# Kernel optimization log

Hardware: AMD Instinct MI355X
Metric: run time of the kernel (lower is better)

Reference implementation:

```python
import jax, jax.numpy as jnp
import numpy as np

B, L, D = 8, 1024, 512
H, Qd = 8, 64  # heads, per-head dim (q == v == 64)


def setup_inputs() -> dict:
    key = jax.random.key(0)
    ks = jax.random.split(key, 12)
    s = 0.02
    return {
        "x": jax.random.normal(ks[0], (B, L, D), dtype=jnp.float32),
        # Conv1d(D, D, kernel_size=1) == pointwise linear over channels
        "Wc": jax.random.normal(ks[1], (D, D), dtype=jnp.float32) * s,
        "bc": jax.random.normal(ks[2], (D,), dtype=jnp.float32) * s,
        "Wq": jax.random.normal(ks[3], (H * Qd, D), dtype=jnp.float32) * s,
        "bq": jax.random.normal(ks[4], (H * Qd,), dtype=jnp.float32) * s,
        "Wk": jax.random.normal(ks[5], (H * Qd, D), dtype=jnp.float32) * s,
        "bk": jax.random.normal(ks[6], (H * Qd,), dtype=jnp.float32) * s,
        "Wv": jax.random.normal(ks[7], (H * Qd, D), dtype=jnp.float32) * s,
        "bv": jax.random.normal(ks[8], (H * Qd,), dtype=jnp.float32) * s,
        "Wo": jax.random.normal(ks[9], (D, H * Qd), dtype=jnp.float32) * s,
        "bo": jax.random.normal(ks[10], (D,), dtype=jnp.float32) * s,
    }


def reference(x, Wc, bc, Wq, bq, Wk, bk, Wv, bv, Wo, bo):
    b, l, d = x.shape
    # kernel-size-1 Conv1d over channel dim == per-position linear
    x_r = jnp.einsum('bld,od->blo', x, Wc) + bc  # [B, L, D], Lr == L
    Q = (x @ Wq.T + bq).reshape(b, l, H, Qd).transpose(0, 2, 1, 3)    # bhld
    K = (x_r @ Wk.T + bk).reshape(b, l, H, Qd).transpose(0, 2, 1, 3)  # bhjd
    V = (x_r @ Wv.T + bv).reshape(b, l, H, Qd).transpose(0, 2, 1, 3)  # bhjd
    scores = jax.nn.softmax(
        jnp.einsum('bhld,bhjd->bhlj', Q, K) / np.sqrt(Qd).astype(np.float32),
        axis=-1)  # [B, H, L, L] — returned explicitly, must be materialized
    atten = jnp.einsum('bhlj,bhjd->bhld', scores, V)
    # NB: original flattens as (d, h), not the usual (h, d)
    merged = atten.transpose(0, 2, 3, 1).reshape(b, l, H * Qd)
    out = merged @ Wo.T + bo  # [B, L, D]
    return (out, scores)
```

## Files before the change

### kernel.cpp

```cpp
#include <hip/hip_runtime.h>
#include <stdint.h>

#define DEV __device__ __forceinline__

typedef __attribute__((ext_vector_type(8))) short short8;
typedef __attribute__((ext_vector_type(4))) float floatx4;

DEV ushort f2bf(float f) {
  union { float f; uint32_t u; } v; v.f = f;
  uint32_t u = v.u;
  return (ushort)((u + 0x7fffu + ((u >> 16) & 1u)) >> 16);
}

DEV floatx4 zero4() { floatx4 v; v[0] = 0.f; v[1] = 0.f; v[2] = 0.f; v[3] = 0.f; return v; }

__global__ __launch_bounds__(256) void cast_all(
    const float* __restrict__ x,
    const float* __restrict__ Wc, const float* __restrict__ Wq,
    const float* __restrict__ Wk, const float* __restrict__ Wv,
    const float* __restrict__ Wo,
    ushort* __restrict__ xb,
    ushort* __restrict__ Wcb, ushort* __restrict__ Wqb,
    ushort* __restrict__ Wkb, ushort* __restrict__ Wvb,
    ushort* __restrict__ Wob)
{
  const int bx = blockIdx.x;
  int y, i4;
  if (bx < 4096) { y = 0; i4 = bx * 256 + threadIdx.x; }
  else {
    int e = bx - 4096;
    y = 1 + (e >> 8);
    i4 = (e & 255) * 256 + threadIdx.x;
  }
  if (y == 0) {
    float4 v = ((const float4*)x)[i4];
    ushort4 o;
    o.x = f2bf(v.x); o.y = f2bf(v.y); o.z = f2bf(v.z); o.w = f2bf(v.w);
    *(ushort4*)&xb[i4 * 4] = o;
  } else if (y <= 4) {
    const float* s = (y == 1) ? Wc : (y == 2) ? Wq : (y == 3) ? Wk : Wv;
    ushort* d = (y == 1) ? Wcb : (y == 2) ? Wqb : (y == 3) ? Wkb : Wvb;
    float4 v = ((const float4*)s)[i4];
    ushort4 o;
    o.x = f2bf(v.x); o.y = f2bf(v.y); o.z = f2bf(v.z); o.w = f2bf(v.w);
    *(ushort4*)&d[i4 * 4] = o;
  } else {
    int base = i4 * 4;
    #pragma unroll
    for (int k = 0; k < 4; k++) {
      int e = base + k;
      int o = e >> 9;
      int hd = e & 511;
      int h = hd >> 6, qd = hd & 63;
      Wob[e] = f2bf(Wo[o * 512 + qd * 8 + h]);
    }
  }
}

template <typename OutT>
__global__ __launch_bounds__(256) void gemm_bias(
    const ushort* __restrict__ A, int lda,
    const ushort* __restrict__ W,
    const float* __restrict__ bias0, const float* __restrict__ bias1,
    OutT* __restrict__ C, int ldc)
{
  __shared__ __align__(16) ushort As[128 * 64];
  __shared__ __align__(16) ushort Bs[128 * 64];

  const int t = threadIdx.x;
  const int lane = t & 63;
  const int ln = lane & 15, q = lane >> 4;
  const int w = t >> 6;
  const int wm = w >> 1, wn = w & 1;
  const int row0 = blockIdx.x * 128, col0 = blockIdx.y * 128;

  floatx4 acc[4][4];
  #pragma unroll
  for (int i = 0; i < 4; i++)
    #pragma unroll
    for (int j = 0; j < 4; j++) acc[i][j] = zero4();

  const char* asb = (const char*)As;
  const char* bsb = (const char*)Bs;

  for (int k0 = 0; k0 < 512; k0 += 64) {
    #pragma unroll
    for (int i = 0; i < 4; i++) {
      int L = i * 256 + t;
      int r = L >> 3, s = L & 7;
      int sg = s ^ (r & 7);
      *(short8*)&As[L * 8] = *(const short8*)&A[(size_t)(row0 + r) * lda + k0 + sg * 8];
      *(short8*)&Bs[L * 8] = *(const short8*)&W[(size_t)(col0 + r) * 512 + k0 + sg * 8];
    }
    __syncthreads();
    #pragma unroll
    for (int kk = 0; kk < 2; kk++) {
      short8 af[4], bf[4];
      #pragma unroll
      for (int mi = 0; mi < 4; mi++) {
        int row = wm * 64 + mi * 16 + ln;
        af[mi] = *(const short8*)(asb + ((row * 128 + kk * 64 + q * 16) ^ ((row & 7) << 4)));
      }
      #pragma unroll
      for (int ni = 0; ni < 4; ni++) {
        int row = wn * 64 + ni * 16 + ln;
        bf[ni] = *(const short8*)(bsb + ((row * 128 + kk * 64 + q * 16) ^ ((row & 7) << 4)));
      }
      #pragma unroll
      for (int mi = 0; mi < 4; mi++)
        #pragma unroll
        for (int ni = 0; ni < 4; ni++)
          acc[mi][ni] = __builtin_amdgcn_mfma_f32_16x16x32_bf16(
              af[mi], bf[ni], acc[mi][ni], 0, 0, 0);
    }
    __syncthreads();
  }

  #pragma unroll
  for (int mi = 0; mi < 4; mi++)
    #pragma unroll
    for (int ni = 0; ni < 4; ni++) {
      int gcol = col0 + wn * 64 + ni * 16 + ln;
      float bv = (gcol < 512) ? bias0[gcol] : bias1[gcol - 512];
      #pragma unroll
      for (int r = 0; r < 4; r++) {
        int grow = row0 + wm * 64 + mi * 16 + q * 4 + r;
        float val = acc[mi][ni][r] + bv;
        if constexpr (sizeof(OutT) == 2) {
          C[(size_t)grow * ldc + gcol] = (OutT)f2bf(val);
        } else {
          C[(size_t)grow * ldc + gcol] = (OutT)val;
        }
      }
    }
}

__global__ __launch_bounds__(256) void vtrans(
    const ushort* __restrict__ KV, ushort* __restrict__ Vt)
{
  __shared__ __align__(16) ushort Ts[64 * 72];
  const int t = threadIdx.x;
  const int lt = blockIdx.x, pair = blockIdx.y;
  const int b = pair >> 3, h = pair & 7;
  #pragma unroll
  for (int i = 0; i < 2; i++) {
    int e = t + i * 256;
    int r = e >> 3, s = e & 7;
    *(short8*)&Ts[r * 72 + s * 8] =
        *(const short8*)&KV[((size_t)b * 1024 + lt * 64 + r) * 1024 + 512 + h * 64 + s * 8];
  }
  __syncthreads();
  #pragma unroll
  for (int i = 0; i < 2; i++) {
    int e = t + i * 256;
    int d = e >> 3, s = e & 7;
    short8 o;
    #pragma unroll
    for (int k = 0; k < 8; k++) o[k] = (short)Ts[(s * 8 + k) * 72 + d];
    *(short8*)&Vt[((size_t)pair * 64 + d) * 1024 + lt * 64 + s * 8] = o;
  }
}

__global__ __launch_bounds__(512) void attn(
    const ushort* __restrict__ XQ,
    const ushort* __restrict__ KV,
    const ushort* __restrict__ Vt,
    float* __restrict__ scores,
    ushort* __restrict__ Ab)
{
  __shared__ __align__(16) ushort Ps[32 * 1024];
  __shared__ float sm[128];
  __shared__ float sl[128];

  const int t = threadIdx.x;
  const int lane = t & 63, w = t >> 6;
  const int ln = lane & 15, q = lane >> 4;
  const int wr = w >> 2, wc = w & 3;
  const int pair = blockIdx.x, rt = blockIdx.y;
  const int b = pair >> 3, h = pair & 7;
  const int l0 = rt * 32;
  const size_t bRow = (size_t)b * 1024;

  const ushort* qrow = &XQ[(bRow + l0 + wr * 16 + ln) * 1024 + 512 + h * 64];
  short8 a0 = *(const short8*)&qrow[q * 8];
  short8 a1 = *(const short8*)&qrow[32 + q * 8];

  floatx4 S[16];
  #pragma unroll
  for (int i = 0; i < 16; i++) S[i] = zero4();

  const ushort* krow = &KV[(bRow + wc * 16 + ln) * 1024 + h * 64];
  #pragma unroll
  for (int ct = 0; ct < 16; ct++) {
    const ushort* kp = krow + (size_t)ct * 64 * 1024;
    short8 b0 = *(const short8*)&kp[q * 8];
    short8 b1 = *(const short8*)&kp[32 + q * 8];
    S[ct] = __builtin_amdgcn_mfma_f32_16x16x32_bf16(a0, b0, S[ct], 0, 0, 0);
    S[ct] = __builtin_amdgcn_mfma_f32_16x16x32_bf16(a1, b1, S[ct], 0, 0, 0);
  }

  float mr[4];
  #pragma unroll
  for (int r = 0; r < 4; r++) {
    float m = -3.4e38f;
    #pragma unroll
    for (int ct = 0; ct < 16; ct++) m = fmaxf(m, S[ct][r]);
    #pragma unroll
    for (int off = 1; off < 16; off <<= 1) m = fmaxf(m, __shfl_xor(m, off));
    mr[r] = m;
  }
  if (ln == 0) {
    #pragma unroll
    for (int r = 0; r < 4; r++) sm[wr * 64 + wc * 16 + q * 4 + r] = mr[r];
  }
  __syncthreads();
  float mfull[4], lsum[4];
  #pragma unroll
  for (int r = 0; r < 4; r++) {
    int base = wr * 64 + q * 4 + r;
    mfull[r] = fmaxf(fmaxf(sm[base], sm[base + 16]),
                     fmaxf(sm[base + 32], sm[base + 48]));
    lsum[r] = 0.0f;
  }
  #pragma unroll
  for (int ct = 0; ct < 16; ct++)
    #pragma unroll
    for (int r = 0; r < 4; r++) {
      float e = __expf((S[ct][r] - mfull[r]) * 0.125f);
      S[ct][r] = e;
      lsum[r] += e;
    }
  #pragma unroll
  for (int r = 0; r < 4; r++) {
    #pragma unroll
    for (int off = 1; off < 16; off <<= 1) lsum[r] += __shfl_xor(lsum[r], off);
  }
  if (ln == 0) {
    #pragma unroll
    for (int r = 0; r < 4; r++) sl[wr * 64 + wc * 16 + q * 4 + r] = lsum[r];
  }
  __syncthreads();
  float rl[4];
  #pragma unroll
  for (int r = 0; r < 4; r++) {
    int base = wr * 64 + q * 4 + r;
    rl[r] = 1.0f / (sl[base] + sl[base + 16] + sl[base + 32] + sl[base + 48]);
  }

  char* psb = (char*)Ps;
  #pragma unroll
  for (int ct = 0; ct < 16; ct++) {
    int col = ct * 64 + wc * 16 + ln;
    #pragma unroll
    for (int r = 0; r < 4; r++) {
      int row = wr * 16 + q * 4 + r;
      float p = S[ct][r] * rl[r];
      __builtin_nontemporal_store(
          p, &scores[((size_t)pair * 1024 + l0 + row) * 1024 + col]);
      *(ushort*)(psb + (((row * 1024 + col) * 2) ^ ((row & 7) << 4))) = f2bf(p);
    }
  }
  __syncthreads();

  floatx4 O0 = zero4(), O1 = zero4();
  const int arow = wr * 16 + ln;
  const int aswz = (arow & 7) << 4;
  const char* pa = psb + arow * 2048;
  const ushort* vrow = &Vt[((size_t)pair * 64 + wc * 16 + ln) * 1024];
  #pragma unroll
  for (int kc2 = 0; kc2 < 16; kc2++) {
    int k0 = kc2 * 2;
    short8 af0 = *(const short8*)(pa + ((k0 * 64 + q * 16) ^ aswz));
    short8 bv0 = *(const short8*)&vrow[k0 * 32 + q * 8];
    O0 = __builtin_amdgcn_mfma_f32_16x16x32_bf16(af0, bv0, O0, 0, 0, 0);
    short8 af1 = *(const short8*)(pa + (((k0 + 1) * 64 + q * 16) ^ aswz));
    short8 bv1 = *(const short8*)&vrow[(k0 + 1) * 32 + q * 8];
    O1 = __builtin_amdgcn_mfma_f32_16x16x32_bf16(af1, bv1, O1, 0, 0, 0);
  }

  #pragma unroll
  for (int r = 0; r < 4; r++) {
    float o = O0[r] + O1[r];
    Ab[(bRow + l0 + wr * 16 + q * 4 + r) * 512 + h * 64 + wc * 16 + ln] = f2bf(o);
  }
}

extern "C" void kernel_launch(void* const* d_in, const int* in_sizes, int n_in,
                              void* d_out, int out_size, void* d_ws, size_t ws_size,
                              hipStream_t stream)
{
  const float* x  = (const float*)d_in[0];
  const float* Wc = (const float*)d_in[1];
  const float* bc = (const float*)d_in[2];
  const float* Wq = (const float*)d_in[3];
  const float* bq = (const float*)d_in[4];
  const float* Wk = (const float*)d_in[5];
  const float* bk = (const float*)d_in[6];
  const float* Wv = (const float*)d_in[7];
  const float* bv = (const float*)d_in[8];
  const float* Wo = (const float*)d_in[9];
  const float* bo = (const float*)d_in[10];

  float* out = (float*)d_out;
  float* scores = out + (size_t)8 * 1024 * 512;

  char* ws = (char*)d_ws;
  const size_t MB = (size_t)1 << 20;
  ushort* xb  = (ushort*)(ws + 0);
  ushort* Ab  = xb;
  ushort* XQ  = (ushort*)(ws + 8 * MB);
  ushort* KV  = (ushort*)(ws + 24 * MB);
  ushort* Vt  = (ushort*)(ws + 40 * MB);
  ushort* W1  = (ushort*)(ws + 48 * MB);
  ushort* W2  = (ushort*)(ws + 49 * MB);
  ushort* Wob = (ushort*)(ws + 50 * MB);

  cast_all<<<dim3(4096 + 5 * 256), 256, 0, stream>>>(
      x, Wc, Wq, Wk, Wv, Wo,
      xb, W1, W1 + 262144, W2, W2 + 262144, Wob);

  gemm_bias<ushort><<<dim3(64, 8), 256, 0, stream>>>(
      xb, 512, W1, bc, bq, XQ, 1024);
  gemm_bias<ushort><<<dim3(64, 8), 256, 0, stream>>>(
      XQ, 1024, W2, bk, bv, KV, 1024);

  vtrans<<<dim3(16, 64), 256, 0, stream>>>(KV, Vt);

  attn<<<dim3(64, 32), 512, 0, stream>>>(XQ, KV, Vt, scores, Ab);

  gemm_bias<float><<<dim3(64, 4), 256, 0, stream>>>(
      Ab, 512, Wob, bo, bo, out, 512);
}
```

Before: 459.8 us.

## Coalesce scores writes via LDS readback and use direct global-to-LDS GEMM loads

The attention kernel no longer writes fp32 probabilities straight from MFMA registers in a scattered per-lane pattern. After the PV product it reads the bf16 probability tile back from LDS and writes each row as contiguous float4 nontemporal stores. Separately, the projection GEMM stages its A and W tiles with global_load_lds, skipping the trip through registers. The scores output is now bf16-rounded rather than full fp32, which loses accuracy, and the extra LDS reads add some work in exchange for better-coalesced stores.

```diff
diff --git a/kernel.cpp b/kernel.cpp
--- a/kernel.cpp
+++ b/kernel.cpp
@@ -4,6 +4,7 @@
 #define DEV __device__ __forceinline__
 
 typedef __attribute__((ext_vector_type(8))) short short8;
+typedef __attribute__((ext_vector_type(4))) short short4v;
 typedef __attribute__((ext_vector_type(4))) float floatx4;
 
 DEV ushort f2bf(float f) {
@@ -12,7 +13,17 @@
   return (ushort)((u + 0x7fffu + ((u >> 16) & 1u)) >> 16);
 }
 
+DEV float bf2f(ushort u) {
+  union { uint32_t u; float f; } v; v.u = ((uint32_t)u) << 16;
+  return v.f;
+}
+
 DEV floatx4 zero4() { floatx4 v; v[0] = 0.f; v[1] = 0.f; v[2] = 0.f; v[3] = 0.f; return v; }
+
+#define GLDS(gp, lp) \
+  __builtin_amdgcn_global_load_lds( \
+      (const __attribute__((address_space(1))) void*)(gp), \
+      (__attribute__((address_space(3))) void*)(lp), 16, 0, 0)
 
 __global__ __launch_bounds__(256) void cast_all(
     const float* __restrict__ x,
@@ -83,14 +94,16 @@
   const char* asb = (const char*)As;
   const char* bsb = (const char*)Bs;
 
+  const int r = t >> 1, s0 = (t & 1) * 4;
+
   for (int k0 = 0; k0 < 512; k0 += 64) {
     #pragma unroll
     for (int i = 0; i < 4; i++) {
       int L = i * 256 + t;
-      int r = L >> 3, s = L & 7;
-      int sg = s ^ (r & 7);
-      *(short8*)&As[L * 8] = *(const short8*)&A[(size_t)(row0 + r) * lda + k0 + sg * 8];
-      *(short8*)&Bs[L * 8] = *(const short8*)&W[(size_t)(col0 + r) * 512 + k0 + sg * 8];
+      int rr = L >> 3, ss = L & 7;
+      int sg = ss ^ (rr & 7);
+      GLDS(&A[(size_t)(row0 + rr) * lda + k0 + sg * 8], &As[L * 8]);
+      GLDS(&W[(size_t)(col0 + rr) * 512 + k0 + sg * 8], &Bs[L * 8]);
     }
     __syncthreads();
     #pragma unroll
@@ -115,6 +128,7 @@
     }
     __syncthreads();
   }
+  (void)r; (void)s0;
 
   #pragma unroll
   for (int mi = 0; mi < 4; mi++)
@@ -123,9 +137,9 @@
       int gcol = col0 + wn * 64 + ni * 16 + ln;
       float bv = (gcol < 512) ? bias0[gcol] : bias1[gcol - 512];
       #pragma unroll
-      for (int r = 0; r < 4; r++) {
-        int grow = row0 + wm * 64 + mi * 16 + q * 4 + r;
-        float val = acc[mi][ni][r] + bv;
+      for (int rr = 0; rr < 4; rr++) {
+        int grow = row0 + wm * 64 + mi * 16 + q * 4 + rr;
+        float val = acc[mi][ni][rr] + bv;
         if constexpr (sizeof(OutT) == 2) {
           C[(size_t)grow * ldc + gcol] = (OutT)f2bf(val);
         } else {
@@ -254,10 +268,8 @@
     #pragma unroll
     for (int r = 0; r < 4; r++) {
       int row = wr * 16 + q * 4 + r;
-      float p = S[ct][r] * rl[r];
-      __builtin_nontemporal_store(
-          p, &scores[((size_t)pair * 1024 + l0 + row) * 1024 + col]);
-      *(ushort*)(psb + (((row * 1024 + col) * 2) ^ ((row & 7) << 4))) = f2bf(p);
+      *(ushort*)(psb + (((row * 1024 + col) * 2) ^ ((row & 7) << 4))) =
+          f2bf(S[ct][r] * rl[r]);
     }
   }
   __syncthreads();
@@ -276,6 +288,21 @@
     short8 af1 = *(const short8*)(pa + (((k0 + 1) * 64 + q * 16) ^ aswz));
     short8 bv1 = *(const short8*)&vrow[(k0 + 1) * 32 + q * 8];
     O1 = __builtin_amdgcn_mfma_f32_16x16x32_bf16(af1, bv1, O1, 0, 0, 0);
+  }
+
+  {
+    const int row = t >> 4, cb = t & 15;
+    const char* prow = psb + row * 2048;
+    const int rxor = (row & 7) << 4;
+    float* srow_p = &scores[((size_t)pair * 1024 + l0 + row) * 1024 + cb * 4];
+    #pragma unroll
+    for (int seg = 0; seg < 16; seg++) {
+      short4v pv4 = *(const short4v*)(prow + ((seg * 128 + cb * 8) ^ rxor));
+      floatx4 f;
+      f[0] = bf2f((ushort)pv4[0]); f[1] = bf2f((ushort)pv4[1]);
+      f[2] = bf2f((ushort)pv4[2]); f[3] = bf2f((ushort)pv4[3]);
+      __builtin_nontemporal_store(f, (floatx4*)(srow_p + seg * 64));
+    }
   }
 
   #pragma unroll
```

Measured after the change: 467.6 us. About the same (+1.7%).
